# Kernel tuning notes

Hardware: AMD Instinct MI355X
Metric: run time of the kernel (lower is better)

The kernel has to match this reference:

```python
import jax, jax.numpy as jnp
import numpy as np
from jax import lax

B, CIN, H, W = 64, 1024, 28, 28
MID, COUT = 256, 1024  # mid_channels, out_channels*expansion
EMB = 64
EPS = 1e-5


def _conv(x, w, stride=1, padding='VALID'):
    return lax.conv_general_dilated(
        x, w, window_strides=(stride, stride), padding=padding,
        dimension_numbers=('NCHW', 'OIHW', 'NCHW'))


def _bn(x, gamma, beta):
    # training-mode BatchNorm2d: batch statistics over (N,H,W)
    m = jnp.mean(x, axis=(0, 2, 3), keepdims=True)
    v = jnp.var(x, axis=(0, 2, 3), keepdims=True)
    return (x - m) * lax.rsqrt(v + EPS) * gamma[None, :, None, None] + beta[None, :, None, None]


def setup_inputs() -> dict:
    key = jax.random.key(0)
    ks = jax.random.split(key, 12)
    he = lambda k, shape, fan_in: jax.random.normal(k, shape, jnp.float32) * np.float32(np.sqrt(2.0 / fan_in))
    return {
        'x': jax.random.normal(ks[0], (B, CIN, H, W), jnp.float32),
        'embeddings': jax.random.normal(ks[1], (B, EMB), jnp.float32),
        # sparse gating networks: Linear(emb_dim -> channels) + ReLU
        'w_gate1': he(ks[2], (EMB, MID), EMB), 'b_gate1': jnp.zeros((MID,), jnp.float32),
        'w_gate2': he(ks[3], (EMB, MID), EMB), 'b_gate2': jnp.zeros((MID,), jnp.float32),
        'conv1_w': he(ks[4], (MID, CIN, 1, 1), CIN),
        'bn1_g': jnp.ones((MID,), jnp.float32), 'bn1_b': jnp.zeros((MID,), jnp.float32),
        'conv2_w': he(ks[5], (MID, MID, 3, 3), MID * 9),
        'bn2_g': jnp.ones((MID,), jnp.float32), 'bn2_b': jnp.zeros((MID,), jnp.float32),
        'conv3_w': he(ks[6], (COUT, MID, 1, 1), MID),
        'bn3_g': jnp.ones((COUT,), jnp.float32), 'bn3_b': jnp.zeros((COUT,), jnp.float32),
    }


def reference(x, embeddings, w_gate1, b_gate1, w_gate2, b_gate2,
              conv1_w, bn1_g, bn1_b, conv2_w, bn2_g, bn2_b,
              conv3_w, bn3_g, bn3_b):
    identity = x
    # gate 1: ReLU-sparse gating over mid channels, per sample
    g1 = jax.nn.relu(embeddings @ w_gate1 + b_gate1)            # [B, MID]
    out = _conv(x, conv1_w) * g1[:, :, None, None]              # MoE conv1x1
    out = jax.nn.relu(_bn(out, bn1_g, bn1_b))
    g2 = jax.nn.relu(embeddings @ w_gate2 + b_gate2)            # [B, MID]
    out = _conv(out, conv2_w, stride=1, padding='SAME') * g2[:, :, None, None]  # MoE conv3x3
    out = jax.nn.relu(_bn(out, bn2_g, bn2_b))
    out = _conv(out, conv3_w)                                   # plain conv1x1
    out = _bn(out, bn3_g, bn3_b)
    out = jax.nn.relu(out + identity)
    return out, g1, g2
```

## Files before the change

### kernel.cpp

```cpp
#include <hip/hip_runtime.h>
#include <stdint.h>

#define NB 64
#define CINC 1024
#define HWD 784
#define MIDC 256
#define COUTC 1024
#define EMBD 64

typedef __attribute__((ext_vector_type(8))) short short8;
typedef __attribute__((ext_vector_type(4))) float f32x4;

#define GLOAD16(gp, lp)                                                     \
  __builtin_amdgcn_global_load_lds(                                         \
      (const __attribute__((address_space(1))) void*)(gp),                  \
      (__attribute__((address_space(3))) void*)(lp), 16, 0, 0)

__device__ __forceinline__ ushort f2bf(float f) {
  union { float f; uint32_t u; } v; v.f = f;
  uint32_t r = v.u + 0x7fffu + ((v.u >> 16) & 1u);
  return (ushort)(r >> 16);
}
__device__ __forceinline__ float bf2f(ushort b) {
  union { uint32_t u; float f; } v; v.u = ((uint32_t)b) << 16;
  return v.f;
}
__device__ __forceinline__ uint32_t pack2(float a, float b) {
  return (uint32_t)f2bf(a) | ((uint32_t)f2bf(b) << 16);
}

static const size_t OFF_Y1   = 0;
static const size_t OFF_Y2   = 25690112;
static const size_t OFF_W1   = 51380224;
static const size_t OFF_W3   = 51904512;
static const size_t OFF_W2R  = 52428800;
static const size_t OFF_STAT = 53608448;
static const size_t OFF_PAR  = 53620736;

__global__ __launch_bounds__(256) void k_gates(
    const float* __restrict__ emb, const float* __restrict__ w1,
    const float* __restrict__ b1, const float* __restrict__ w2,
    const float* __restrict__ b2, float* __restrict__ out_tail) {
  int b = blockIdx.x, which = blockIdx.y, n = threadIdx.x;
  const float* w = which ? w2 : w1;
  const float* bias = which ? b2 : b1;
  __shared__ float se[EMBD];
  if (n < EMBD) se[n] = emb[b * EMBD + n];
  __syncthreads();
  float acc = bias[n];
#pragma unroll 8
  for (int e = 0; e < EMBD; e++) acc += se[e] * w[e * MIDC + n];
  acc = fmaxf(acc, 0.f);
  out_tail[which * (NB * MIDC) + b * MIDC + n] = acc;
}

__global__ void k_repack(const float* __restrict__ w1, const float* __restrict__ w2,
                         const float* __restrict__ w3, ushort* __restrict__ W1b,
                         ushort* __restrict__ W2r, ushort* __restrict__ W3b) {
  int total = 262144 + 262144 + 589824;
  for (int i = blockIdx.x * blockDim.x + threadIdx.x; i < total;
       i += gridDim.x * blockDim.x) {
    if (i < 262144) W1b[i] = f2bf(w1[i]);
    else if (i < 524288) W3b[i - 262144] = f2bf(w3[i - 262144]);
    else {
      int j = i - 524288;
      int tap = j >> 16, n = (j >> 8) & 255, c = j & 255;
      W2r[j] = f2bf(w2[(n * 256 + c) * 9 + tap]);
    }
  }
}

__global__ __launch_bounds__(256) void k_xpose(const float* __restrict__ x,
                                               ushort* __restrict__ xcl) {
  int mt = blockIdx.x, ct = blockIdx.y, b = blockIdx.z;
  __shared__ float tile[64][68];
  int t = threadIdx.x;
  int m0 = mt * 64, c0 = ct * 64;
  {
    int cc = t >> 2, mc = (t & 3) << 4;
    if (m0 + mc < HWD) {
      const float* src = x + ((size_t)b * CINC + c0 + cc) * HWD + m0 + mc;
#pragma unroll
      for (int e = 0; e < 4; e++) {
        float4 q = ((const float4*)src)[e];
        int mm = mc + e * 4;
        tile[mm][cc] = q.x; tile[mm + 1][cc] = q.y;
        tile[mm + 2][cc] = q.z; tile[mm + 3][cc] = q.w;
      }
    }
  }
  __syncthreads();
  {
    int m = t >> 2, cc = (t & 3) << 4;
    int mi = m0 + m;
    if (mi < HWD) {
      float* row = tile[m];
      uint32_t w[8];
#pragma unroll
      for (int e = 0; e < 8; e++) w[e] = pack2(row[cc + 2 * e], row[cc + 2 * e + 1]);
      uint4 p0, p1;
      p0.x = w[0]; p0.y = w[1]; p0.z = w[2]; p0.w = w[3];
      p1.x = w[4]; p1.y = w[5]; p1.z = w[6]; p1.w = w[7];
      uint4* dst = (uint4*)(xcl + ((size_t)b * HWD + mi) * CINC + c0 + cc);
      dst[0] = p0; dst[1] = p1;
    }
  }
}

__global__ __launch_bounds__(256, 3) void k_conv1(
    const ushort* __restrict__ xcl, const ushort* __restrict__ W1b,
    const float* __restrict__ g1, ushort* __restrict__ y1,
    float* __restrict__ sum1, float* __restrict__ sq1) {
  int bid = blockIdx.x;
  int mt = bid >> 1, nt = bid & 1;
  int tid = threadIdx.x, lane = tid & 63, wid = tid >> 6;
  int wm = wid >> 1, wn = wid & 1;
  int lr = lane & 15, lq = lane >> 4;
  __shared__ char smem[32768];
  char* Ab = smem;
  char* Bb = smem + 16384;

  int l8 = lane >> 3, kgl = lane & 7;
  int xorg = (kgl ^ l8) * 8;
  const ushort* srcA[4]; const ushort* srcB[4];
#pragma unroll
  for (int q = 0; q < 4; q++) {
    int r = (wid * 4 + q) * 8 + l8;
    int m = mt * 128 + r;
    srcA[q] = xcl + (size_t)m * CINC + xorg;
    int n = nt * 128 + r;
    srcB[q] = W1b + (size_t)n * CINC + xorg;
  }
  f32x4 acc[4][4] = {};

  for (int kt = 0; kt < 16; kt++) {
    int d = kt * 64;
#pragma unroll
    for (int q = 0; q < 4; q++) GLOAD16(srcA[q] + d, Ab + (wid * 4 + q) * 1024);
#pragma unroll
    for (int q = 0; q < 4; q++) GLOAD16(srcB[q] + d, Bb + (wid * 4 + q) * 1024);
    __syncthreads();
#pragma unroll
    for (int kk = 0; kk < 2; kk++) {
      int kg = kk * 4 + lq;
      short8 af[4], bf[4];
#pragma unroll
      for (int i = 0; i < 4; i++) {
        int row = wm * 64 + i * 16 + lr;
        af[i] = *(const short8*)(Ab + row * 128 + ((kg ^ (row & 7)) << 4));
      }
#pragma unroll
      for (int j = 0; j < 4; j++) {
        int rn = wn * 64 + j * 16 + lr;
        bf[j] = *(const short8*)(Bb + rn * 128 + ((kg ^ (rn & 7)) << 4));
      }
#pragma unroll
      for (int i = 0; i < 4; i++)
#pragma unroll
        for (int j = 0; j < 4; j++)
          acc[i][j] = __builtin_amdgcn_mfma_f32_16x16x32_bf16(af[i], bf[j], acc[i][j], 0, 0, 0);
    }
    __syncthreads();
  }

  int m0t = mt * 128;
  int b0 = m0t / HWD;
  int b1 = b0 + 1; if (b1 > NB - 1) b1 = NB - 1;
  int thr = (b0 + 1) * HWD;
  float gv0[4], gv1[4];
#pragma unroll
  for (int j = 0; j < 4; j++) {
    int n = nt * 128 + wn * 64 + j * 16 + lr;
    gv0[j] = g1[b0 * MIDC + n];
    gv1[j] = g1[b1 * MIDC + n];
  }
#pragma unroll
  for (int i = 0; i < 4; i++) {
    int mlb = m0t + wm * 64 + i * 16 + lq * 4;
#pragma unroll
    for (int j = 0; j < 4; j++)
#pragma unroll
      for (int r = 0; r < 4; r++)
        acc[i][j][r] *= ((mlb + r) < thr) ? gv0[j] : gv1[j];
  }
#pragma unroll
  for (int j = 0; j < 4; j++) {
    float s = 0.f, q = 0.f;
#pragma unroll
    for (int i = 0; i < 4; i++)
#pragma unroll
      for (int r = 0; r < 4; r++) { float v = acc[i][j][r]; s += v; q += v * v; }
    s += __shfl_xor(s, 16); s += __shfl_xor(s, 32);
    q += __shfl_xor(q, 16); q += __shfl_xor(q, 32);
    if (lane < 16) {
      int n = nt * 128 + wn * 64 + j * 16 + lane;
      atomicAdd(&sum1[n], s); atomicAdd(&sq1[n], q);
    }
  }
#pragma unroll
  for (int i = 0; i < 4; i++)
#pragma unroll
    for (int r = 0; r < 4; r++) {
      int m = m0t + wm * 64 + i * 16 + lq * 4 + r;
      ushort* dst = y1 + (size_t)m * MIDC + nt * 128 + wn * 64 + lr;
#pragma unroll
      for (int j = 0; j < 4; j++) dst[j * 16] = f2bf(acc[i][j][r]);
    }
}

__global__ void k_bnpar(const float* __restrict__ st, const float* __restrict__ gamma,
                        const float* __restrict__ beta, float* __restrict__ so,
                        float* __restrict__ to, int C) {
  int c = blockIdx.x * blockDim.x + threadIdx.x;
  if (c >= C) return;
  const float cnt = 50176.f;
  float m = st[c] / cnt;
  float v = st[C + c] / cnt - m * m;
  float s = gamma[c] * rsqrtf(v + 1e-5f);
  so[c] = s; to[c] = beta[c] - m * s;
}

__global__ __launch_bounds__(256) void k_bnrelu(
    const ushort* __restrict__ y1, const float* __restrict__ s1,
    const float* __restrict__ t1, ushort* __restrict__ y1p) {
  __shared__ float sS[MIDC], sT[MIDC];
  int t = threadIdx.x;
  sS[t] = s1[t]; sT[t] = t1[t];
  __syncthreads();
  int pl = t >> 5, ch = (t & 31) * 8;
  int pos = blockIdx.x * 8 + pl;
  int b = pos / 900, pp = pos % 900;
  int pr = pp / 30, pc = pp % 30;
  uint4 ov = {0u, 0u, 0u, 0u};
  if (pr > 0 && pr < 29 && pc > 0 && pc < 29) {
    uint4 raw = *(const uint4*)(y1 + ((size_t)b * HWD + (pr - 1) * 28 + (pc - 1)) * MIDC + ch);
    ushort* rw = (ushort*)&raw; ushort* ow = (ushort*)&ov;
#pragma unroll
    for (int e = 0; e < 8; e++) {
      float f = bf2f(rw[e]) * sS[ch + e] + sT[ch + e];
      ow[e] = f2bf(fmaxf(f, 0.f));
    }
  }
  *(uint4*)(y1p + (size_t)pos * MIDC + ch) = ov;
}

__global__ __launch_bounds__(256) void k_bnrelu2(
    const ushort* __restrict__ y2, const float* __restrict__ s2,
    const float* __restrict__ t2, ushort* __restrict__ y2p) {
  __shared__ float sS[MIDC], sT[MIDC];
  int t = threadIdx.x;
  sS[t] = s2[t]; sT[t] = t2[t];
  __syncthreads();
  int pl = t >> 5, ch = (t & 31) * 8;
  size_t pos = (size_t)blockIdx.x * 8 + pl;
  uint4 raw = *(const uint4*)(y2 + pos * MIDC + ch);
  uint4 ov;
  ushort* rw = (ushort*)&raw; ushort* ow = (ushort*)&ov;
#pragma unroll
  for (int e = 0; e < 8; e++) {
    float f = bf2f(rw[e]) * sS[ch + e] + sT[ch + e];
    ow[e] = f2bf(fmaxf(f, 0.f));
  }
  *(uint4*)(y2p + pos * MIDC + ch) = ov;
}

__global__ __launch_bounds__(256, 3) void k_conv2(
    const ushort* __restrict__ y1p, const ushort* __restrict__ W2r,
    const float* __restrict__ g2, ushort* __restrict__ y2,
    float* __restrict__ sum2, float* __restrict__ sq2) {
  int bid = blockIdx.x;
  int mt = bid >> 1, nt = bid & 1;
  int tid = threadIdx.x, lane = tid & 63, wid = tid >> 6;
  int wm = wid >> 1, wn = wid & 1;
  int lr = lane & 15, lq = lane >> 4;
  __shared__ char smem[32768];
  char* Ab = smem;
  char* Bb = smem + 16384;

  int l8 = lane >> 3, kgl = lane & 7;
  int xorg = (kgl ^ l8) * 8;
  const ushort* srcA[4]; const ushort* srcB[4];
#pragma unroll
  for (int q = 0; q < 4; q++) {
    int r = (wid * 4 + q) * 8 + l8;
    int m = mt * 128 + r;
    int b = m / HWD, rem = m % HWD;
    int h = rem / 28, w = rem % 28;
    srcA[q] = y1p + ((size_t)b * 900 + (h + 1) * 30 + (w + 1)) * MIDC + xorg;
    int n = nt * 128 + r;
    srcB[q] = W2r + (size_t)n * MIDC + xorg;
  }
  f32x4 acc[4][4] = {};

  for (int kt = 0; kt < 36; kt++) {
    int tap = kt >> 2, cq = kt & 3;
    int dy = tap / 3, dx = tap % 3;
    int dA = ((dy - 1) * 30 + (dx - 1)) * MIDC + cq * 64;
    int dB = tap * 65536 + cq * 64;
#pragma unroll
    for (int q = 0; q < 4; q++) GLOAD16(srcA[q] + dA, Ab + (wid * 4 + q) * 1024);
#pragma unroll
    for (int q = 0; q < 4; q++) GLOAD16(srcB[q] + dB, Bb + (wid * 4 + q) * 1024);
    __syncthreads();
#pragma unroll
    for (int kk = 0; kk < 2; kk++) {
      int kg = kk * 4 + lq;
      short8 af[4], bf[4];
#pragma unroll
      for (int i = 0; i < 4; i++) {
        int row = wm * 64 + i * 16 + lr;
        af[i] = *(const short8*)(Ab + row * 128 + ((kg ^ (row & 7)) << 4));
      }
#pragma unroll
      for (int j = 0; j < 4; j++) {
        int rn = wn * 64 + j * 16 + lr;
        bf[j] = *(const short8*)(Bb + rn * 128 + ((kg ^ (rn & 7)) << 4));
      }
#pragma unroll
      for (int i = 0; i < 4; i++)
#pragma unroll
        for (int j = 0; j < 4; j++)
          acc[i][j] = __builtin_amdgcn_mfma_f32_16x16x32_bf16(af[i], bf[j], acc[i][j], 0, 0, 0);
    }
    __syncthreads();
  }

  int m0t = mt * 128;
  int b0 = m0t / HWD;
  int b1 = b0 + 1; if (b1 > NB - 1) b1 = NB - 1;
  int thr = (b0 + 1) * HWD;
  float gv0[4], gv1[4];
#pragma unroll
  for (int j = 0; j < 4; j++) {
    int n = nt * 128 + wn * 64 + j * 16 + lr;
    gv0[j] = g2[b0 * MIDC + n];
    gv1[j] = g2[b1 * MIDC + n];
  }
#pragma unroll
  for (int i = 0; i < 4; i++) {
    int mlb = m0t + wm * 64 + i * 16 + lq * 4;
#pragma unroll
    for (int j = 0; j < 4; j++)
#pragma unroll
      for (int r = 0; r < 4; r++)
        acc[i][j][r] *= ((mlb + r) < thr) ? gv0[j] : gv1[j];
  }
#pragma unroll
  for (int j = 0; j < 4; j++) {
    float s = 0.f, q = 0.f;
#pragma unroll
    for (int i = 0; i < 4; i++)
#pragma unroll
      for (int r = 0; r < 4; r++) { float v = acc[i][j][r]; s += v; q += v * v; }
    s += __shfl_xor(s, 16); s += __shfl_xor(s, 32);
    q += __shfl_xor(q, 16); q += __shfl_xor(q, 32);
    if (lane < 16) {
      int n = nt * 128 + wn * 64 + j * 16 + lane;
      atomicAdd(&sum2[n], s); atomicAdd(&sq2[n], q);
    }
  }
#pragma unroll
  for (int i = 0; i < 4; i++)
#pragma unroll
    for (int r = 0; r < 4; r++) {
      int m = m0t + wm * 64 + i * 16 + lq * 4 + r;
      ushort* dst = y2 + (size_t)m * MIDC + nt * 128 + wn * 64 + lr;
#pragma unroll
      for (int j = 0; j < 4; j++) dst[j * 16] = f2bf(acc[i][j][r]);
    }
}

__global__ __launch_bounds__(256, 3) void k_conv3(
    const ushort* __restrict__ y2p, const ushort* __restrict__ W3b,
    float* __restrict__ z, float* __restrict__ sum3, float* __restrict__ sq3) {
  int bid = blockIdx.x;
  int mt = bid >> 3, nt = bid & 7;
  int tid = threadIdx.x, lane = tid & 63, wid = tid >> 6;
  int wm = wid >> 1, wn = wid & 1;
  int lr = lane & 15, lq = lane >> 4;
  __shared__ char smem[33792];
  char* Ab = smem;
  char* Bb = smem + 16384;

  int l8 = lane >> 3, kgl = lane & 7;
  int xorg = (kgl ^ l8) * 8;
  const ushort* srcA[4]; const ushort* srcB[4];
#pragma unroll
  for (int q = 0; q < 4; q++) {
    int r = (wid * 4 + q) * 8 + l8;
    int m = mt * 128 + r;
    srcA[q] = y2p + (size_t)m * MIDC + xorg;
    int n = nt * 128 + r;
    srcB[q] = W3b + (size_t)n * MIDC + xorg;
  }
  f32x4 acc[4][4] = {};

  for (int kt = 0; kt < 4; kt++) {
    int d = kt * 64;
#pragma unroll
    for (int q = 0; q < 4; q++) GLOAD16(srcA[q] + d, Ab + (wid * 4 + q) * 1024);
#pragma unroll
    for (int q = 0; q < 4; q++) GLOAD16(srcB[q] + d, Bb + (wid * 4 + q) * 1024);
    __syncthreads();
#pragma unroll
    for (int kk = 0; kk < 2; kk++) {
      int kg = kk * 4 + lq;
      short8 af[4], bf[4];
#pragma unroll
      for (int i = 0; i < 4; i++) {
        int row = wm * 64 + i * 16 + lr;
        af[i] = *(const short8*)(Ab + row * 128 + ((kg ^ (row & 7)) << 4));
      }
#pragma unroll
      for (int j = 0; j < 4; j++) {
        int rn = wn * 64 + j * 16 + lr;
        bf[j] = *(const short8*)(Bb + rn * 128 + ((kg ^ (rn & 7)) << 4));
      }
#pragma unroll
      for (int i = 0; i < 4; i++)
#pragma unroll
        for (int j = 0; j < 4; j++)
          acc[i][j] = __builtin_amdgcn_mfma_f32_16x16x32_bf16(af[i], bf[j], acc[i][j], 0, 0, 0);
    }
    __syncthreads();
  }

#pragma unroll
  for (int j = 0; j < 4; j++) {
    float s = 0.f, q = 0.f;
#pragma unroll
    for (int i = 0; i < 4; i++)
#pragma unroll
      for (int r = 0; r < 4; r++) { float v = acc[i][j][r]; s += v; q += v * v; }
    s += __shfl_xor(s, 16); s += __shfl_xor(s, 32);
    q += __shfl_xor(q, 16); q += __shfl_xor(q, 32);
    if (lane < 16) {
      int n = nt * 128 + wn * 64 + j * 16 + lane;
      atomicAdd(&sum3[n], s); atomicAdd(&sq3[n], q);
    }
  }

  float* ldsf = (float*)smem;
  int m0t = mt * 128;
  for (int h = 0; h < 2; h++) {
    __syncthreads();
    if (wn == h) {
#pragma unroll
      for (int i = 0; i < 4; i++)
#pragma unroll
        for (int j = 0; j < 4; j++) {
          int nc = j * 16 + lr;
#pragma unroll
          for (int r = 0; r < 4; r++) {
            int m = wm * 64 + i * 16 + lq * 4 + r;
            ldsf[nc * 132 + m] = acc[i][j][r];
          }
        }
    }
    __syncthreads();
    int nl = tid >> 2, mc = (tid & 3) * 32;
    int c = nt * 128 + h * 64 + nl;
#pragma unroll
    for (int c4 = 0; c4 < 8; c4++) {
      int m = m0t + mc + c4 * 4;
      int b = m / HWD, hw = m % HWD;
      float4 v = *(const float4*)&ldsf[nl * 132 + mc + c4 * 4];
      *(float4*)(z + ((size_t)(b * COUTC + c)) * HWD + hw) = v;
    }
  }
}

__global__ __launch_bounds__(256) void k_final(
    const float* __restrict__ x, float* __restrict__ z,
    const float* __restrict__ s3, const float* __restrict__ t3) {
  int stride = gridDim.x * blockDim.x;
  int total = (NB * COUTC * HWD) / 4;
  for (int i = blockIdx.x * blockDim.x + threadIdx.x; i < total; i += stride) {
    uint32_t e0 = (uint32_t)i << 2;
    int c = (int)((e0 / HWD) & (COUTC - 1));
    float4 zv = ((const float4*)z)[i];
    float4 xv = ((const float4*)x)[i];
    float s = s3[c], tt = t3[c];
    float4 o;
    o.x = fmaxf(fmaf(zv.x, s, tt) + xv.x, 0.f);
    o.y = fmaxf(fmaf(zv.y, s, tt) + xv.y, 0.f);
    o.z = fmaxf(fmaf(zv.z, s, tt) + xv.z, 0.f);
    o.w = fmaxf(fmaf(zv.w, s, tt) + xv.w, 0.f);
    ((float4*)z)[i] = o;
  }
}

extern "C" void kernel_launch(void* const* d_in, const int* in_sizes, int n_in,
                              void* d_out, int out_size, void* d_ws, size_t ws_size,
                              hipStream_t stream) {
  const float* x    = (const float*)d_in[0];
  const float* emb  = (const float*)d_in[1];
  const float* wg1  = (const float*)d_in[2];
  const float* bg1  = (const float*)d_in[3];
  const float* wg2  = (const float*)d_in[4];
  const float* bg2  = (const float*)d_in[5];
  const float* c1w  = (const float*)d_in[6];
  const float* bn1g = (const float*)d_in[7];
  const float* bn1b = (const float*)d_in[8];
  const float* c2w  = (const float*)d_in[9];
  const float* bn2g = (const float*)d_in[10];
  const float* bn2b = (const float*)d_in[11];
  const float* c3w  = (const float*)d_in[12];
  const float* bn3g = (const float*)d_in[13];
  const float* bn3b = (const float*)d_in[14];

  float* out = (float*)d_out;
  char* ws = (char*)d_ws;
  ushort* y1  = (ushort*)(ws + OFF_Y1);
  ushort* y2p = (ushort*)(ws + OFF_Y1);
  ushort* y2  = (ushort*)(ws + OFF_Y2);
  ushort* W1b = (ushort*)(ws + OFF_W1);
  ushort* W3b = (ushort*)(ws + OFF_W3);
  ushort* W2r = (ushort*)(ws + OFF_W2R);
  float* stat = (float*)(ws + OFF_STAT);
  float* par  = (float*)(ws + OFF_PAR);

  float* sum1 = stat;        float* sq1 = stat + 256;
  float* sum2 = stat + 512;  float* sq2 = stat + 768;
  float* sum3 = stat + 1024; float* sq3 = stat + 2048;
  float* s1 = par;        float* t1 = par + 256;
  float* s2 = par + 512;  float* t2 = par + 768;
  float* s3 = par + 1024; float* t3 = par + 2048;

  ushort* xcl = (ushort*)out;
  ushort* y1p = (ushort*)(out + 25690112);
  float* zbuf = out;
  float* out_tail = out + 51380224;

  hipMemsetAsync(stat, 0, 3072 * sizeof(float), stream);
  k_gates<<<dim3(64, 2), 256, 0, stream>>>(emb, wg1, bg1, wg2, bg2, out_tail);
  k_repack<<<2048, 256, 0, stream>>>(c1w, c2w, c3w, W1b, W2r, W3b);
  k_xpose<<<dim3(13, 16, 64), 256, 0, stream>>>(x, xcl);
  k_conv1<<<784, 256, 0, stream>>>(xcl, W1b, out_tail, y1, sum1, sq1);
  k_bnpar<<<1, 256, 0, stream>>>(stat, bn1g, bn1b, s1, t1, 256);
  k_bnrelu<<<7200, 256, 0, stream>>>(y1, s1, t1, y1p);
  k_conv2<<<784, 256, 0, stream>>>(y1p, W2r, out_tail + 16384, y2, sum2, sq2);
  k_bnpar<<<1, 256, 0, stream>>>(stat + 512, bn2g, bn2b, s2, t2, 256);
  k_bnrelu2<<<6272, 256, 0, stream>>>(y2, s2, t2, y2p);
  k_conv3<<<3136, 256, 0, stream>>>(y2p, W3b, zbuf, sum3, sq3);
  k_bnpar<<<4, 256, 0, stream>>>(stat + 1024, bn3g, bn3b, s3, t3, 1024);
  k_final<<<4096, 256, 0, stream>>>(x, zbuf, s3, t3);
}
```

Before: 455.6 us.

## Store conv3 output as bf16 channels-last and transpose in final epilogue

conv3 now writes its pre-BN result as bf16 in channels-last layout to a workspace buffer, dropping the LDS transpose and the fp32 NCHW store. The final kernel reads the bf16 tiles, applies the BN scale and shift, transposes through LDS and adds the residual while writing fp32 NCHW output. This roughly halves the intermediate traffic for the largest tensor. Block indices in the three conv kernels are also remapped so that consecutive blocks are spread across the 8 XCDs, which may improve L2 locality. The cost is an extra bf16 rounding of the conv3 output before BN, plus strided 2-byte scattered stores in the conv3 epilogue.

```diff
diff --git a/kernel.cpp b/kernel.cpp
--- a/kernel.cpp
+++ b/kernel.cpp
@@ -36,6 +36,7 @@
 static const size_t OFF_W2R  = 52428800;
 static const size_t OFF_STAT = 53608448;
 static const size_t OFF_PAR  = 53620736;
+static const size_t OFF_ZB   = 58720256;
 
 __global__ __launch_bounds__(256) void k_gates(
     const float* __restrict__ emb, const float* __restrict__ w1,
@@ -111,7 +112,7 @@
     const ushort* __restrict__ xcl, const ushort* __restrict__ W1b,
     const float* __restrict__ g1, ushort* __restrict__ y1,
     float* __restrict__ sum1, float* __restrict__ sq1) {
-  int bid = blockIdx.x;
+  int bid = (blockIdx.x & 7) * 98 + (blockIdx.x >> 3);
   int mt = bid >> 1, nt = bid & 1;
   int tid = threadIdx.x, lane = tid & 63, wid = tid >> 6;
   int wm = wid >> 1, wn = wid & 1;
@@ -268,7 +269,7 @@
     const ushort* __restrict__ y1p, const ushort* __restrict__ W2r,
     const float* __restrict__ g2, ushort* __restrict__ y2,
     float* __restrict__ sum2, float* __restrict__ sq2) {
-  int bid = blockIdx.x;
+  int bid = (blockIdx.x & 7) * 98 + (blockIdx.x >> 3);
   int mt = bid >> 1, nt = bid & 1;
   int tid = threadIdx.x, lane = tid & 63, wid = tid >> 6;
   int wm = wid >> 1, wn = wid & 1;
@@ -372,13 +373,13 @@
 
 __global__ __launch_bounds__(256, 3) void k_conv3(
     const ushort* __restrict__ y2p, const ushort* __restrict__ W3b,
-    float* __restrict__ z, float* __restrict__ sum3, float* __restrict__ sq3) {
-  int bid = blockIdx.x;
+    ushort* __restrict__ zb, float* __restrict__ sum3, float* __restrict__ sq3) {
+  int bid = (blockIdx.x & 7) * 392 + (blockIdx.x >> 3);
   int mt = bid >> 3, nt = bid & 7;
   int tid = threadIdx.x, lane = tid & 63, wid = tid >> 6;
   int wm = wid >> 1, wn = wid & 1;
   int lr = lane & 15, lq = lane >> 4;
-  __shared__ char smem[33792];
+  __shared__ char smem[32768];
   char* Ab = smem;
   char* Bb = smem + 16384;
 
@@ -440,53 +441,62 @@
     }
   }
 
-  float* ldsf = (float*)smem;
   int m0t = mt * 128;
-  for (int h = 0; h < 2; h++) {
-    __syncthreads();
-    if (wn == h) {
-#pragma unroll
-      for (int i = 0; i < 4; i++)
-#pragma unroll
-        for (int j = 0; j < 4; j++) {
-          int nc = j * 16 + lr;
-#pragma unroll
-          for (int r = 0; r < 4; r++) {
-            int m = wm * 64 + i * 16 + lq * 4 + r;
-            ldsf[nc * 132 + m] = acc[i][j][r];
-          }
-        }
-    }
-    __syncthreads();
-    int nl = tid >> 2, mc = (tid & 3) * 32;
-    int c = nt * 128 + h * 64 + nl;
-#pragma unroll
-    for (int c4 = 0; c4 < 8; c4++) {
-      int m = m0t + mc + c4 * 4;
-      int b = m / HWD, hw = m % HWD;
-      float4 v = *(const float4*)&ldsf[nl * 132 + mc + c4 * 4];
-      *(float4*)(z + ((size_t)(b * COUTC + c)) * HWD + hw) = v;
-    }
-  }
+#pragma unroll
+  for (int i = 0; i < 4; i++)
+#pragma unroll
+    for (int r = 0; r < 4; r++) {
+      int m = m0t + wm * 64 + i * 16 + lq * 4 + r;
+      ushort* dst = zb + (size_t)m * COUTC + nt * 128 + wn * 64 + lr;
+#pragma unroll
+      for (int j = 0; j < 4; j++) dst[j * 16] = f2bf(acc[i][j][r]);
+    }
 }
 
 __global__ __launch_bounds__(256) void k_final(
-    const float* __restrict__ x, float* __restrict__ z,
-    const float* __restrict__ s3, const float* __restrict__ t3) {
-  int stride = gridDim.x * blockDim.x;
-  int total = (NB * COUTC * HWD) / 4;
-  for (int i = blockIdx.x * blockDim.x + threadIdx.x; i < total; i += stride) {
-    uint32_t e0 = (uint32_t)i << 2;
-    int c = (int)((e0 / HWD) & (COUTC - 1));
-    float4 zv = ((const float4*)z)[i];
-    float4 xv = ((const float4*)x)[i];
-    float s = s3[c], tt = t3[c];
-    float4 o;
-    o.x = fmaxf(fmaf(zv.x, s, tt) + xv.x, 0.f);
-    o.y = fmaxf(fmaf(zv.y, s, tt) + xv.y, 0.f);
-    o.z = fmaxf(fmaf(zv.z, s, tt) + xv.z, 0.f);
-    o.w = fmaxf(fmaf(zv.w, s, tt) + xv.w, 0.f);
-    ((float4*)z)[i] = o;
+    const ushort* __restrict__ zb, const float* __restrict__ x,
+    const float* __restrict__ s3, const float* __restrict__ t3,
+    float* __restrict__ outp) {
+  int ht = blockIdx.x, ct = blockIdx.y, b = blockIdx.z;
+  __shared__ float tile[64][65];
+  __shared__ float sS[64], sT[64];
+  int t = threadIdx.x;
+  if (t < 64) { sS[t] = s3[ct * 64 + t]; sT[t] = t3[ct * 64 + t]; }
+  __syncthreads();
+  int hw0 = ht * 64;
+  {
+    int hwl = t >> 2, cl = (t & 3) * 16;
+    int hw = hw0 + hwl;
+    if (hw < HWD) {
+      const ushort* src = zb + ((size_t)b * HWD + hw) * COUTC + ct * 64 + cl;
+      uint4 r0 = ((const uint4*)src)[0], r1 = ((const uint4*)src)[1];
+      ushort* w0 = (ushort*)&r0; ushort* w1 = (ushort*)&r1;
+#pragma unroll
+      for (int e = 0; e < 8; e++)
+        tile[hwl][cl + e] = bf2f(w0[e]) * sS[cl + e] + sT[cl + e];
+#pragma unroll
+      for (int e = 0; e < 8; e++)
+        tile[hwl][cl + 8 + e] = bf2f(w1[e]) * sS[cl + 8 + e] + sT[cl + 8 + e];
+    }
+  }
+  __syncthreads();
+  {
+    int cl = t >> 2, hwl = (t & 3) * 16;
+    int c = ct * 64 + cl;
+    size_t base = ((size_t)b * COUTC + c) * HWD;
+#pragma unroll
+    for (int e4 = 0; e4 < 4; e4++) {
+      int hwv = hw0 + hwl + e4 * 4;
+      if (hwv < HWD) {
+        float4 xv = *(const float4*)(x + base + hwv);
+        float4 o;
+        o.x = fmaxf(tile[hwl + e4 * 4 + 0][cl] + xv.x, 0.f);
+        o.y = fmaxf(tile[hwl + e4 * 4 + 1][cl] + xv.y, 0.f);
+        o.z = fmaxf(tile[hwl + e4 * 4 + 2][cl] + xv.z, 0.f);
+        o.w = fmaxf(tile[hwl + e4 * 4 + 3][cl] + xv.w, 0.f);
+        *(float4*)(outp + base + hwv) = o;
+      }
+    }
   }
 }
 
@@ -519,6 +529,7 @@
   ushort* W2r = (ushort*)(ws + OFF_W2R);
   float* stat = (float*)(ws + OFF_STAT);
   float* par  = (float*)(ws + OFF_PAR);
+  ushort* zb  = (ushort*)(ws + OFF_ZB);
 
   float* sum1 = stat;        float* sq1 = stat + 256;
   float* sum2 = stat + 512;  float* sq2 = stat + 768;
@@ -529,7 +540,6 @@
 
   ushort* xcl = (ushort*)out;
   ushort* y1p = (ushort*)(out + 25690112);
-  float* zbuf = out;
   float* out_tail = out + 51380224;
 
   hipMemsetAsync(stat, 0, 3072 * sizeof(float), stream);
@@ -542,7 +552,7 @@
   k_conv2<<<784, 256, 0, stream>>>(y1p, W2r, out_tail + 16384, y2, sum2, sq2);
   k_bnpar<<<1, 256, 0, stream>>>(stat + 512, bn2g, bn2b, s2, t2, 256);
   k_bnrelu2<<<6272, 256, 0, stream>>>(y2, s2, t2, y2p);
-  k_conv3<<<3136, 256, 0, stream>>>(y2p, W3b, zbuf, sum3, sq3);
+  k_conv3<<<3136, 256, 0, stream>>>(y2p, W3b, zb, sum3, sq3);
   k_bnpar<<<4, 256, 0, stream>>>(stat + 1024, bn3g, bn3b, s3, t3, 1024);
-  k_final<<<4096, 256, 0, stream>>>(x, zbuf, s3, t3);
-}
+  k_final<<<dim3(13, 16, 64), 256, 0, stream>>>(zb, x, s3, t3, out);
+}
```

Measured after the change: 546.1 us. 1.2x slower.

## Store conv3 output as bf16 in workspace and remap block order for XCD locality

Applied to the files above, without the earlier changes.

The conv3 pre-BN output is now written as bf16 into a separate workspace buffer instead of fp32 into the output buffer, and the final BN+residual+ReLU kernel reads the bf16 values and writes fp32 to the output. This roughly halves the bytes written by conv3 and read back by the final pass. Block indices in all three conv kernels are also permuted so that consecutive tiles land on the same XCD, which improves L2 reuse of the shared A/B operands. The cost is an extra bf16 rounding of the pre-normalization activations, while the BN statistics are still computed from the fp32 accumulators.

```diff
diff --git a/kernel.cpp b/kernel.cpp
--- a/kernel.cpp
+++ b/kernel.cpp
@@ -36,6 +36,7 @@
 static const size_t OFF_W2R  = 52428800;
 static const size_t OFF_STAT = 53608448;
 static const size_t OFF_PAR  = 53620736;
+static const size_t OFF_ZB   = 58720256;
 
 __global__ __launch_bounds__(256) void k_gates(
     const float* __restrict__ emb, const float* __restrict__ w1,
@@ -111,7 +112,7 @@
     const ushort* __restrict__ xcl, const ushort* __restrict__ W1b,
     const float* __restrict__ g1, ushort* __restrict__ y1,
     float* __restrict__ sum1, float* __restrict__ sq1) {
-  int bid = blockIdx.x;
+  int bid = (blockIdx.x & 7) * 98 + (blockIdx.x >> 3);
   int mt = bid >> 1, nt = bid & 1;
   int tid = threadIdx.x, lane = tid & 63, wid = tid >> 6;
   int wm = wid >> 1, wn = wid & 1;
@@ -268,7 +269,7 @@
     const ushort* __restrict__ y1p, const ushort* __restrict__ W2r,
     const float* __restrict__ g2, ushort* __restrict__ y2,
     float* __restrict__ sum2, float* __restrict__ sq2) {
-  int bid = blockIdx.x;
+  int bid = (blockIdx.x & 7) * 98 + (blockIdx.x >> 3);
   int mt = bid >> 1, nt = bid & 1;
   int tid = threadIdx.x, lane = tid & 63, wid = tid >> 6;
   int wm = wid >> 1, wn = wid & 1;
@@ -372,8 +373,8 @@
 
 __global__ __launch_bounds__(256, 3) void k_conv3(
     const ushort* __restrict__ y2p, const ushort* __restrict__ W3b,
-    float* __restrict__ z, float* __restrict__ sum3, float* __restrict__ sq3) {
-  int bid = blockIdx.x;
+    ushort* __restrict__ zbn, float* __restrict__ sum3, float* __restrict__ sq3) {
+  int bid = (blockIdx.x & 7) * 392 + (blockIdx.x >> 3);
   int mt = bid >> 3, nt = bid & 7;
   int tid = threadIdx.x, lane = tid & 63, wid = tid >> 6;
   int wm = wid >> 1, wn = wid & 1;
@@ -458,35 +459,47 @@
         }
     }
     __syncthreads();
-    int nl = tid >> 2, mc = (tid & 3) * 32;
-    int c = nt * 128 + h * 64 + nl;
-#pragma unroll
-    for (int c4 = 0; c4 < 8; c4++) {
-      int m = m0t + mc + c4 * 4;
-      int b = m / HWD, hw = m % HWD;
-      float4 v = *(const float4*)&ldsf[nl * 132 + mc + c4 * 4];
-      *(float4*)(z + ((size_t)(b * COUTC + c)) * HWD + hw) = v;
+    int c0 = nt * 128 + h * 64;
+    int l = tid & 15;
+    int m = m0t + l * 8;
+    int b = m / HWD, hw = m % HWD;
+#pragma unroll
+    for (int pass = 0; pass < 4; pass++) {
+      int row = pass * 16 + (tid >> 4);
+      const float* src = &ldsf[row * 132 + l * 8];
+      uint4 pv;
+      pv.x = pack2(src[0], src[1]); pv.y = pack2(src[2], src[3]);
+      pv.z = pack2(src[4], src[5]); pv.w = pack2(src[6], src[7]);
+      *(uint4*)(zbn + ((size_t)(b * COUTC + c0 + row)) * HWD + hw) = pv;
     }
   }
 }
 
 __global__ __launch_bounds__(256) void k_final(
-    const float* __restrict__ x, float* __restrict__ z,
-    const float* __restrict__ s3, const float* __restrict__ t3) {
+    const ushort* __restrict__ zbn, const float* __restrict__ x,
+    const float* __restrict__ s3, const float* __restrict__ t3,
+    float* __restrict__ outp) {
   int stride = gridDim.x * blockDim.x;
-  int total = (NB * COUTC * HWD) / 4;
+  int total = (NB * COUTC * HWD) / 8;
   for (int i = blockIdx.x * blockDim.x + threadIdx.x; i < total; i += stride) {
-    uint32_t e0 = (uint32_t)i << 2;
+    size_t e0 = (size_t)i * 8;
     int c = (int)((e0 / HWD) & (COUTC - 1));
-    float4 zv = ((const float4*)z)[i];
-    float4 xv = ((const float4*)x)[i];
     float s = s3[c], tt = t3[c];
-    float4 o;
-    o.x = fmaxf(fmaf(zv.x, s, tt) + xv.x, 0.f);
-    o.y = fmaxf(fmaf(zv.y, s, tt) + xv.y, 0.f);
-    o.z = fmaxf(fmaf(zv.z, s, tt) + xv.z, 0.f);
-    o.w = fmaxf(fmaf(zv.w, s, tt) + xv.w, 0.f);
-    ((float4*)z)[i] = o;
+    uint4 zr = *(const uint4*)(zbn + e0);
+    ushort* zw = (ushort*)&zr;
+    float4 x0 = *(const float4*)(x + e0);
+    float4 x1 = *(const float4*)(x + e0 + 4);
+    float4 o0, o1;
+    o0.x = fmaxf(fmaf(bf2f(zw[0]), s, tt) + x0.x, 0.f);
+    o0.y = fmaxf(fmaf(bf2f(zw[1]), s, tt) + x0.y, 0.f);
+    o0.z = fmaxf(fmaf(bf2f(zw[2]), s, tt) + x0.z, 0.f);
+    o0.w = fmaxf(fmaf(bf2f(zw[3]), s, tt) + x0.w, 0.f);
+    o1.x = fmaxf(fmaf(bf2f(zw[4]), s, tt) + x1.x, 0.f);
+    o1.y = fmaxf(fmaf(bf2f(zw[5]), s, tt) + x1.y, 0.f);
+    o1.z = fmaxf(fmaf(bf2f(zw[6]), s, tt) + x1.z, 0.f);
+    o1.w = fmaxf(fmaf(bf2f(zw[7]), s, tt) + x1.w, 0.f);
+    *(float4*)(outp + e0) = o0;
+    *(float4*)(outp + e0 + 4) = o1;
   }
 }
 
@@ -519,6 +532,7 @@
   ushort* W2r = (ushort*)(ws + OFF_W2R);
   float* stat = (float*)(ws + OFF_STAT);
   float* par  = (float*)(ws + OFF_PAR);
+  ushort* zbn = (ushort*)(ws + OFF_ZB);
 
   float* sum1 = stat;        float* sq1 = stat + 256;
   float* sum2 = stat + 512;  float* sq2 = stat + 768;
@@ -529,7 +543,6 @@
 
   ushort* xcl = (ushort*)out;
   ushort* y1p = (ushort*)(out + 25690112);
-  float* zbuf = out;
   float* out_tail = out + 51380224;
 
   hipMemsetAsync(stat, 0, 3072 * sizeof(float), stream);
@@ -542,7 +555,7 @@
   k_conv2<<<784, 256, 0, stream>>>(y1p, W2r, out_tail + 16384, y2, sum2, sq2);
   k_bnpar<<<1, 256, 0, stream>>>(stat + 512, bn2g, bn2b, s2, t2, 256);
   k_bnrelu2<<<6272, 256, 0, stream>>>(y2, s2, t2, y2p);
-  k_conv3<<<3136, 256, 0, stream>>>(y2p, W3b, zbuf, sum3, sq3);
+  k_conv3<<<3136, 256, 0, stream>>>(y2p, W3b, zbn, sum3, sq3);
   k_bnpar<<<4, 256, 0, stream>>>(stat + 1024, bn3g, bn3b, s3, t3, 1024);
-  k_final<<<4096, 256, 0, stream>>>(x, zbuf, s3, t3);
-}
+  k_final<<<2048, 256, 0, stream>>>(zbn, x, s3, t3, out);
+}
```

Result: faster. 388.2 us, median of 2 (-14.8%).
